# Kernel optimization log

Hardware: AMD Instinct MI355X
Metric: run time of the kernel (lower is better)

## Reference

```python
import jax, jax.numpy as jnp
import numpy as np

B, N, K_OUT, NBASIS, NGLOBALS, H = 16, 2048, 128, 4, 2, 256
DIN = 1 + NBASIS + N + NGLOBALS  # norm + basis projections + all-pairs dots + globals
NEG_SLOPE = 0.01  # torch LeakyReLU default


def setup_inputs() -> dict:
    key = jax.random.key(0)
    ks = jax.random.split(key, 6)
    x = jax.random.uniform(ks[0], (B, N, 3), jnp.float32)      # positions -> dots >= 0
    u = jax.random.normal(ks[1], (B, NGLOBALS), jnp.float32)
    basis = jax.random.normal(ks[2], (B, NBASIS, 3), jnp.float32)
    def init_w(k, fan_in, fan_out):
        return jax.random.normal(k, (fan_in, fan_out), jnp.float32) / np.float32(np.sqrt(fan_in))
    W1 = init_w(ks[3], DIN, H); b1 = jnp.zeros((H,), jnp.float32)
    W2 = init_w(ks[4], H, H);   b2 = jnp.zeros((H,), jnp.float32)
    W3 = init_w(ks[5], H, K_OUT); b3 = jnp.zeros((K_OUT,), jnp.float32)
    return {"x": x, "u": u, "basis": basis,
            "W1": W1, "b1": b1, "W2": W2, "b2": b2, "W3": W3, "b3": b3}


def reference(x, u, basis, W1, b1, W2, b2, W3, b3):
    # per-vector norms: [B, N, 1]
    norms = jnp.linalg.norm(x, axis=-1, keepdims=True)
    # projections onto basis vectors: [B, N, NBASIS]
    proj = jnp.einsum('bid,bnd->bin', x, basis)
    # all-pairs sqrt of dot products: [B, N, N]
    dots = jnp.sqrt(jnp.einsum('bid,bjd->bij', x, x))
    # concat order matches original: globals first, then [norm, proj, dots]
    u_rep = jnp.broadcast_to(u[:, None, :], (B, N, NGLOBALS))
    scalars = jnp.concatenate([u_rep, norms, proj, dots], axis=-1)  # [B, N, DIN]
    # MLP (Linear -> LeakyReLU -> Linear -> LeakyReLU -> Linear)
    h = jax.nn.leaky_relu(scalars @ W1 + b1, NEG_SLOPE)
    h = jax.nn.leaky_relu(h @ W2 + b2, NEG_SLOPE)
    fk = h @ W3 + b3  # [B, N, K_OUT]
    # outer product with x followed by mean over input vecs, fused into one einsum
    # (avoids materializing the [B, N, K_OUT, 3] tensor)
    return jnp.einsum('bio,bid->bod', fk, x) / np.float32(N)  # [B, K_OUT, 3]
```

## Files before the change

### kernel.cpp

```cpp
#include <hip/hip_runtime.h>

typedef unsigned short u16;
typedef unsigned int   u32;

typedef __attribute__((ext_vector_type(8))) short short8;
typedef __attribute__((ext_vector_type(4))) float floatx4;
typedef __attribute__((ext_vector_type(2))) float v2f;

__device__ __forceinline__ u16 f2bf(float f) {
    u32 u = __float_as_uint(f);
    u = u + 0x7fffu + ((u >> 16) & 1u);
    return (u16)(u >> 16);
}

__device__ __forceinline__ u32 pack2bf(float s0, float s1) {
    u32 a = __float_as_uint(s0) + 0x8000u;
    u32 b = __float_as_uint(s1) + 0x8000u;
    return __builtin_amdgcn_perm(b, a, 0x07060302u);
}

__device__ __forceinline__ floatx4 mfma16(short8 a, short8 b, floatx4 c) {
    return __builtin_amdgcn_mfma_f32_16x16x32_bf16(a, b, c, 0, 0, 0);
}

__global__ void k_prep(const float* __restrict__ W1, const float* __restrict__ W2,
                       const float* __restrict__ W3, u16* __restrict__ W1frag,
                       u16* __restrict__ W2frag, u16* __restrict__ W3frag) {
    int idx = blockIdx.x * 256 + threadIdx.x;
    if (idx < 524288) {
        int kt = idx >> 13, r = idx & 8191;
        int t = r >> 4, j = (r >> 3) & 1, ji = r & 7;
        int lane = t & 63, w = t >> 6, lr = lane & 15, lq = lane >> 4;
        W1frag[idx] = f2bf(W1[(7 + kt * 32 + lq * 8 + ji) * 256 + w * 32 + j * 16 + lr]);
    } else if (idx < 589824) {
        int i = idx - 524288;
        int kt = i >> 13, r = i & 8191;
        int t = r >> 5, jj = (r >> 3) & 3, ji = r & 7;
        int lane = t & 63, wv = t >> 6, lr = lane & 15, lq = lane >> 4;
        W2frag[i] = f2bf(W2[(kt * 32 + lq * 8 + ji) * 256 + wv * 64 + jj * 16 + lr]);
    } else if (idx < 622592) {
        int i = idx - 589824;
        int kt = i >> 12, r = i & 4095;
        int t = r >> 4, j = (r >> 3) & 1, ji = r & 7;
        int lane = t & 63, wv = t >> 6, lr = lane & 15, lq = lane >> 4;
        W3frag[i] = f2bf(W3[(kt * 32 + lq * 8 + ji) * 128 + wv * 32 + j * 16 + lr]);
    }
}

__global__ __launch_bounds__(512, 4) void k_h1(
    const float* __restrict__ x, const float* __restrict__ u,
    const float* __restrict__ basis, const float* __restrict__ W1,
    const float* __restrict__ b1, const u16* __restrict__ W1frag,
    u16* __restrict__ h1) {
    __shared__ float xls[6144];
    __shared__ u16 As[2][64][64];
    __shared__ float rowsml[64][6];
    __shared__ float colsml[256][6];

    const int t = threadIdx.x;
    const int b = blockIdx.y;
    const int i0 = blockIdx.x * 64;
    const int lane = t & 63, w = t >> 6;
    const int lr = lane & 15, lq = lane >> 4;

    {
        const float4* src = (const float4*)(x + b * 6144);
#pragma unroll
        for (int kk = 0; kk < 3; ++kk) {
            int q = t + kk * 512;
            float4 v = src[q];
            float vv[4] = {v.x, v.y, v.z, v.w};
            int e = q * 4;
#pragma unroll
            for (int cc = 0; cc < 4; ++cc) {
                int ee = e + cc;
                xls[(ee % 3) * 2048 + ee / 3] = vv[cc];
            }
        }
    }
    if (t < 256) {
        int c = t;
        float u0 = u[b * 2 + 0], u1 = u[b * 2 + 1];
        colsml[c][0] = b1[c] + u0 * W1[c] + u1 * W1[256 + c];
        colsml[c][1] = W1[512 + c];
        colsml[c][2] = W1[768 + c];
        colsml[c][3] = W1[1024 + c];
        colsml[c][4] = W1[1280 + c];
        colsml[c][5] = W1[1536 + c];
    }
    __syncthreads();
    if (t < 64) {
        float xx = xls[i0 + t], xy = xls[2048 + i0 + t], xz = xls[4096 + i0 + t];
        rowsml[t][0] = sqrtf(xx * xx + xy * xy + xz * xz);
#pragma unroll
        for (int p = 0; p < 4; ++p) {
            const float* bp = basis + (b * 4 + p) * 3;
            rowsml[t][1 + p] = xx * bp[0] + xy * bp[1] + xz * bp[2];
        }
    }
    const float ax = xls[i0 + lane];
    const float ay = xls[2048 + i0 + lane];
    const float az = xls[4096 + i0 + lane];
    const u16* wf = W1frag + t * 16;
    const float4* X4 = (const float4*)xls;

    char* Asb = (char*)As;
    char* aswp = Asb + lane * 128 + ((w ^ (lane & 7)) << 4);
    int ro[4];
    {
        int sl = (lq ^ (lr & 7));
#pragma unroll
        for (int i = 0; i < 4; ++i)
            ro[i] = (i * 16 + lr) * 128 + (sl << 4);
    }

    auto gen_store = [&](int s, int buf) {
        int q = s * 16 + w * 2;
        v2f dA, dB, dC, dD;
        {
            float4 a0 = X4[q], a1 = X4[q + 1];
            v2f t0 = {a0.x, a0.y}, t1 = {a0.z, a0.w};
            v2f t2 = {a1.x, a1.y}, t3 = {a1.z, a1.w};
            dA = t0 * ax; dB = t1 * ax; dC = t2 * ax; dD = t3 * ax;
        }
        {
            float4 a0 = X4[512 + q], a1 = X4[513 + q];
            v2f t0 = {a0.x, a0.y}, t1 = {a0.z, a0.w};
            v2f t2 = {a1.x, a1.y}, t3 = {a1.z, a1.w};
            dA += t0 * ay; dB += t1 * ay; dC += t2 * ay; dD += t3 * ay;
        }
        {
            float4 a0 = X4[1024 + q], a1 = X4[1025 + q];
            v2f t0 = {a0.x, a0.y}, t1 = {a0.z, a0.w};
            v2f t2 = {a1.x, a1.y}, t3 = {a1.z, a1.w};
            dA += t0 * az; dB += t1 * az; dC += t2 * az; dD += t3 * az;
        }
        float s0 = __builtin_amdgcn_sqrtf(dA.x);
        float s1 = __builtin_amdgcn_sqrtf(dA.y);
        float s2 = __builtin_amdgcn_sqrtf(dB.x);
        float s3 = __builtin_amdgcn_sqrtf(dB.y);
        float s4 = __builtin_amdgcn_sqrtf(dC.x);
        float s5 = __builtin_amdgcn_sqrtf(dC.y);
        float s6 = __builtin_amdgcn_sqrtf(dD.x);
        float s7 = __builtin_amdgcn_sqrtf(dD.y);
        uint4 dv;
        dv.x = pack2bf(s0, s1); dv.y = pack2bf(s2, s3);
        dv.z = pack2bf(s4, s5); dv.w = pack2bf(s6, s7);
        *(uint4*)(aswp + buf * 8192) = dv;
    };

    floatx4 acc[4][2];
    const floatx4 zero = {0.f, 0.f, 0.f, 0.f};
#pragma unroll
    for (int i = 0; i < 4; ++i)
#pragma unroll
        for (int j = 0; j < 2; ++j) acc[i][j] = zero;

    gen_store(0, 0);
    __syncthreads();

    short8 a[4], bfr[4];
#pragma unroll 2
    for (int s = 0; s < 32; ++s) {
        const int buf = s & 1;
        const u16* wb = wf + (2 * s) * 8192;
        bfr[0] = *(const short8*)(wb);
        bfr[1] = *(const short8*)(wb + 8);
        bfr[2] = *(const short8*)(wb + 8192);
        bfr[3] = *(const short8*)(wb + 8192 + 8);
#pragma unroll
        for (int i = 0; i < 4; ++i)
            a[i] = *(const short8*)(Asb + buf * 8192 + ro[i]);
        if (s < 31) gen_store(s + 1, buf ^ 1);
#pragma unroll
        for (int i = 0; i < 4; ++i)
#pragma unroll
            for (int j = 0; j < 2; ++j)
                acc[i][j] = mfma16(a[i], bfr[j], acc[i][j]);
#pragma unroll
        for (int i = 0; i < 4; ++i)
            a[i] = *(const short8*)(Asb + buf * 8192 + (ro[i] ^ 64));
#pragma unroll
        for (int i = 0; i < 4; ++i)
#pragma unroll
            for (int j = 0; j < 2; ++j)
                acc[i][j] = mfma16(a[i], bfr[2 + j], acc[i][j]);
        __syncthreads();
    }

    const int c0 = w * 32 + lr, c1 = c0 + 16;
    float c0v[6], c1v[6];
#pragma unroll
    for (int q = 0; q < 6; ++q) { c0v[q] = colsml[c0][q]; c1v[q] = colsml[c1][q]; }
#pragma unroll
    for (int i = 0; i < 4; ++i) {
#pragma unroll
        for (int r = 0; r < 4; ++r) {
            int row = i * 16 + lq * 4 + r;
            float nrm = rowsml[row][0];
            float p0 = rowsml[row][1], p1 = rowsml[row][2];
            float p2 = rowsml[row][3], p3 = rowsml[row][4];
            u16* orow = h1 + (b * 2048 + i0 + row) * 256;
            float v0 = acc[i][0][r] + c0v[0] + nrm * c0v[1] +
                       p0 * c0v[2] + p1 * c0v[3] + p2 * c0v[4] + p3 * c0v[5];
            v0 = v0 > 0.f ? v0 : 0.01f * v0;
            orow[c0] = f2bf(v0);
            float v1 = acc[i][1][r] + c1v[0] + nrm * c1v[1] +
                       p0 * c1v[2] + p1 * c1v[3] + p2 * c1v[4] + p3 * c1v[5];
            v1 = v1 > 0.f ? v1 : 0.01f * v1;
            orow[c1] = f2bf(v1);
        }
    }
}

__global__ __launch_bounds__(256, 2) void k_tail(
    const u16* __restrict__ h1, const u16* __restrict__ W2frag,
    const float* __restrict__ b2, const u16* __restrict__ W3frag,
    const float* __restrict__ b3, const float* __restrict__ x,
    float* __restrict__ out) {
    __shared__ u16 h2s[64][264];
    __shared__ float colb2[256];
    __shared__ float colb3[128];
    __shared__ float xs[64][4];
    __shared__ float red[128][4];

    const int t = threadIdx.x;
    const int m0 = blockIdx.x * 64;
    const int b = m0 >> 11, i0 = m0 & 2047;
    const int lane = t & 63, wv = t >> 6;
    const int lr = lane & 15, lq = lane >> 4;

    colb2[t] = b2[t];
    if (t < 128) colb3[t] = b3[t];
    if (t < 64) {
        const float* xp = x + (b * 2048 + i0 + t) * 3;
        xs[t][0] = xp[0]; xs[t][1] = xp[1]; xs[t][2] = xp[2];
    }

    floatx4 acc[4][4];
    const floatx4 zero = {0.f, 0.f, 0.f, 0.f};
#pragma unroll
    for (int i = 0; i < 4; ++i)
#pragma unroll
        for (int j = 0; j < 4; ++j) acc[i][j] = zero;

    const u16* hsrc = h1 + m0 * 256 + lr * 256 + lq * 8;
    const u16* w2s = W2frag + t * 32;
#pragma unroll 2
    for (int kt = 0; kt < 8; ++kt) {
        short8 af[4], bf[4];
#pragma unroll
        for (int i = 0; i < 4; ++i)
            af[i] = *(const short8*)(hsrc + i * 4096 + kt * 32);
#pragma unroll
        for (int j = 0; j < 4; ++j)
            bf[j] = *(const short8*)(w2s + kt * 8192 + j * 8);
#pragma unroll
        for (int i = 0; i < 4; ++i)
#pragma unroll
            for (int j = 0; j < 4; ++j) acc[i][j] = mfma16(af[i], bf[j], acc[i][j]);
    }
#pragma unroll
    for (int i = 0; i < 4; ++i)
#pragma unroll
        for (int r = 0; r < 4; ++r) {
            int row = i * 16 + lq * 4 + r;
#pragma unroll
            for (int j = 0; j < 4; ++j) {
                int col = wv * 64 + j * 16 + lr;
                float v = acc[i][j][r] + colb2[col];
                v = v > 0.f ? v : 0.01f * v;
                h2s[row][col] = f2bf(v);
            }
        }
    __syncthreads();

    floatx4 acc2[4][2];
#pragma unroll
    for (int i = 0; i < 4; ++i)
#pragma unroll
        for (int j = 0; j < 2; ++j) acc2[i][j] = zero;

    const u16* w3s = W3frag + t * 16;
#pragma unroll 2
    for (int kt = 0; kt < 8; ++kt) {
        short8 af[4], bf[2];
#pragma unroll
        for (int i = 0; i < 4; ++i)
            af[i] = *(const short8*)&h2s[i * 16 + lr][kt * 32 + lq * 8];
#pragma unroll
        for (int j = 0; j < 2; ++j)
            bf[j] = *(const short8*)(w3s + kt * 4096 + j * 8);
#pragma unroll
        for (int i = 0; i < 4; ++i)
#pragma unroll
            for (int j = 0; j < 2; ++j) acc2[i][j] = mfma16(af[i], bf[j], acc2[i][j]);
    }

    float s[2][3];
#pragma unroll
    for (int j = 0; j < 2; ++j) { s[j][0] = 0.f; s[j][1] = 0.f; s[j][2] = 0.f; }
#pragma unroll
    for (int i = 0; i < 4; ++i)
#pragma unroll
        for (int r = 0; r < 4; ++r) {
            int row = i * 16 + lq * 4 + r;
            float x0 = xs[row][0], x1 = xs[row][1], x2 = xs[row][2];
#pragma unroll
            for (int j = 0; j < 2; ++j) {
                int col = wv * 32 + j * 16 + lr;
                float fk = acc2[i][j][r] + colb3[col];
                s[j][0] += fk * x0; s[j][1] += fk * x1; s[j][2] += fk * x2;
            }
        }
#pragma unroll
    for (int j = 0; j < 2; ++j)
#pragma unroll
        for (int d = 0; d < 3; ++d) {
            float v = s[j][d];
            v += __shfl_xor(v, 16);
            v += __shfl_xor(v, 32);
            if (lane < 16) red[wv * 32 + j * 16 + lane][d] = v;
        }
    __syncthreads();
    if (t < 128) {
#pragma unroll
        for (int d = 0; d < 3; ++d)
            atomicAdd(&out[(b * 128 + t) * 3 + d], red[t][d] * (1.0f / 2048.0f));
    }
}

extern "C" void kernel_launch(void* const* d_in, const int* in_sizes, int n_in,
                              void* d_out, int out_size, void* d_ws, size_t ws_size,
                              hipStream_t stream) {
    const float* x     = (const float*)d_in[0];
    const float* u     = (const float*)d_in[1];
    const float* basis = (const float*)d_in[2];
    const float* W1    = (const float*)d_in[3];
    const float* b1    = (const float*)d_in[4];
    const float* W2    = (const float*)d_in[5];
    const float* b2    = (const float*)d_in[6];
    const float* W3    = (const float*)d_in[7];
    const float* b3    = (const float*)d_in[8];
    float* out = (float*)d_out;

    char* ws = (char*)d_ws;
    u16*  W1frag = (u16*)ws;
    u16*  W2frag = (u16*)(ws + 1048576);
    u16*  W3frag = (u16*)(ws + 1179648);
    u16*  h1     = (u16*)(ws + 1245184);

    hipMemsetAsync(out, 0, 24576, stream);
    k_prep<<<2432, 256, 0, stream>>>(W1, W2, W3, W1frag, W2frag, W3frag);
    k_h1<<<dim3(32, 16), 512, 0, stream>>>(x, u, basis, W1, b1, W1frag, h1);
    k_tail<<<512, 256, 0, stream>>>(h1, W2frag, b2, W3frag, b3, x, out);
}
```

Baseline: 137.6 us.

## Fuse layer-1 and tail MLP kernels, keeping h1 in shared memory

Merges the h1 kernel and the tail kernel into one kernel. The 64x256 h1 tile now stays in LDS (aliased over the x staging buffer) and feeds the W2 and W3 GEMMs directly, so the bf16 h1 global round-trip and a kernel launch go away. W2/W3 fragment layouts are re-tiled for 8 waves of 512 threads. LDS use grows to about 76KB per block, which may reduce occupancy below the launch-bounds target. The column constants are now read from global memory per thread instead of staged in LDS.

```diff
diff --git a/kernel.cpp b/kernel.cpp
--- a/kernel.cpp
+++ b/kernel.cpp
@@ -35,27 +35,33 @@
     } else if (idx < 589824) {
         int i = idx - 524288;
         int kt = i >> 13, r = i & 8191;
-        int t = r >> 5, jj = (r >> 3) & 3, ji = r & 7;
-        int lane = t & 63, wv = t >> 6, lr = lane & 15, lq = lane >> 4;
-        W2frag[i] = f2bf(W2[(kt * 32 + lq * 8 + ji) * 256 + wv * 64 + jj * 16 + lr]);
+        int t = r >> 4, j = (r >> 3) & 1, ji = r & 7;
+        int lane = t & 63, w = t >> 6, lr = lane & 15, lq = lane >> 4;
+        W2frag[i] = f2bf(W2[(kt * 32 + lq * 8 + ji) * 256 + w * 32 + j * 16 + lr]);
     } else if (idx < 622592) {
         int i = idx - 589824;
         int kt = i >> 12, r = i & 4095;
-        int t = r >> 4, j = (r >> 3) & 1, ji = r & 7;
-        int lane = t & 63, wv = t >> 6, lr = lane & 15, lq = lane >> 4;
-        W3frag[i] = f2bf(W3[(kt * 32 + lq * 8 + ji) * 128 + wv * 32 + j * 16 + lr]);
-    }
-}
-
-__global__ __launch_bounds__(512, 4) void k_h1(
+        int t = r >> 3, ji = r & 7;
+        int lane = t & 63, w = t >> 6, lr = lane & 15, lq = lane >> 4;
+        W3frag[i] = f2bf(W3[(kt * 32 + lq * 8 + ji) * 128 + w * 16 + lr]);
+    }
+}
+
+__global__ __launch_bounds__(512, 4) void k_fused(
     const float* __restrict__ x, const float* __restrict__ u,
     const float* __restrict__ basis, const float* __restrict__ W1,
-    const float* __restrict__ b1, const u16* __restrict__ W1frag,
-    u16* __restrict__ h1) {
-    __shared__ float xls[6144];
-    __shared__ u16 As[2][64][64];
-    __shared__ float rowsml[64][6];
-    __shared__ float colsml[256][6];
+    const float* __restrict__ b1, const float* __restrict__ b2,
+    const float* __restrict__ b3, const u16* __restrict__ W1frag,
+    const u16* __restrict__ W2frag, const u16* __restrict__ W3frag,
+    float* __restrict__ out) {
+    __shared__ __align__(16) char smem[76288];
+    float* xls = (float*)smem;
+    char* Asb = smem + 24576;
+    u16 (*h1s)[264] = (u16(*)[264])smem;
+    float (*xsm)[4] = (float(*)[4])(smem + 33792);
+    float (*redm)[4] = (float(*)[4])(smem + 34816);
+    float (*rowsml)[6] = (float(*)[6])(smem + 40960);
+    u16 (*h2s)[264] = (u16(*)[264])(smem + 42496);
 
     const int t = threadIdx.x;
     const int b = blockIdx.y;
@@ -78,16 +84,6 @@
             }
         }
     }
-    if (t < 256) {
-        int c = t;
-        float u0 = u[b * 2 + 0], u1 = u[b * 2 + 1];
-        colsml[c][0] = b1[c] + u0 * W1[c] + u1 * W1[256 + c];
-        colsml[c][1] = W1[512 + c];
-        colsml[c][2] = W1[768 + c];
-        colsml[c][3] = W1[1024 + c];
-        colsml[c][4] = W1[1280 + c];
-        colsml[c][5] = W1[1536 + c];
-    }
     __syncthreads();
     if (t < 64) {
         float xx = xls[i0 + t], xy = xls[2048 + i0 + t], xz = xls[4096 + i0 + t];
@@ -104,7 +100,6 @@
     const u16* wf = W1frag + t * 16;
     const float4* X4 = (const float4*)xls;
 
-    char* Asb = (char*)As;
     char* aswp = Asb + lane * 128 + ((w ^ (lane & 7)) << 4);
     int ro[4];
     {
@@ -159,174 +154,147 @@
     gen_store(0, 0);
     __syncthreads();
 
-    short8 a[4], bfr[4];
+    {
+        short8 a[4], bfr[4];
 #pragma unroll 2
-    for (int s = 0; s < 32; ++s) {
-        const int buf = s & 1;
-        const u16* wb = wf + (2 * s) * 8192;
-        bfr[0] = *(const short8*)(wb);
-        bfr[1] = *(const short8*)(wb + 8);
-        bfr[2] = *(const short8*)(wb + 8192);
-        bfr[3] = *(const short8*)(wb + 8192 + 8);
+        for (int s = 0; s < 32; ++s) {
+            const int buf = s & 1;
+            const u16* wb = wf + (2 * s) * 8192;
+            bfr[0] = *(const short8*)(wb);
+            bfr[1] = *(const short8*)(wb + 8);
+            bfr[2] = *(const short8*)(wb + 8192);
+            bfr[3] = *(const short8*)(wb + 8192 + 8);
+#pragma unroll
+            for (int i = 0; i < 4; ++i)
+                a[i] = *(const short8*)(Asb + buf * 8192 + ro[i]);
+            if (s < 31) gen_store(s + 1, buf ^ 1);
+#pragma unroll
+            for (int i = 0; i < 4; ++i)
+#pragma unroll
+                for (int j = 0; j < 2; ++j)
+                    acc[i][j] = mfma16(a[i], bfr[j], acc[i][j]);
+#pragma unroll
+            for (int i = 0; i < 4; ++i)
+                a[i] = *(const short8*)(Asb + buf * 8192 + (ro[i] ^ 64));
+#pragma unroll
+            for (int i = 0; i < 4; ++i)
+#pragma unroll
+                for (int j = 0; j < 2; ++j)
+                    acc[i][j] = mfma16(a[i], bfr[2 + j], acc[i][j]);
+            __syncthreads();
+        }
+    }
+
+    if (t < 64) { xsm[t][0] = ax; xsm[t][1] = ay; xsm[t][2] = az; }
+    const int c0 = w * 32 + lr, c1 = c0 + 16;
+    {
+        float c0v[6], c1v[6];
+        float u0 = u[b * 2 + 0], u1 = u[b * 2 + 1];
+        c0v[0] = b1[c0] + u0 * W1[c0] + u1 * W1[256 + c0];
+        c1v[0] = b1[c1] + u0 * W1[c1] + u1 * W1[256 + c1];
+#pragma unroll
+        for (int q = 1; q < 6; ++q) {
+            c0v[q] = W1[(q + 1) * 256 + c0];
+            c1v[q] = W1[(q + 1) * 256 + c1];
+        }
+#pragma unroll
+        for (int i = 0; i < 4; ++i) {
+#pragma unroll
+            for (int r = 0; r < 4; ++r) {
+                int row = i * 16 + lq * 4 + r;
+                float nrm = rowsml[row][0];
+                float p0 = rowsml[row][1], p1 = rowsml[row][2];
+                float p2 = rowsml[row][3], p3 = rowsml[row][4];
+                float v0 = acc[i][0][r] + c0v[0] + nrm * c0v[1] +
+                           p0 * c0v[2] + p1 * c0v[3] + p2 * c0v[4] + p3 * c0v[5];
+                v0 = v0 > 0.f ? v0 : 0.01f * v0;
+                h1s[row][c0] = f2bf(v0);
+                float v1 = acc[i][1][r] + c1v[0] + nrm * c1v[1] +
+                           p0 * c1v[2] + p1 * c1v[3] + p2 * c1v[4] + p3 * c1v[5];
+                v1 = v1 > 0.f ? v1 : 0.01f * v1;
+                h1s[row][c1] = f2bf(v1);
+            }
+        }
+    }
+    __syncthreads();
+
+#pragma unroll
+    for (int i = 0; i < 4; ++i)
+#pragma unroll
+        for (int j = 0; j < 2; ++j) acc[i][j] = zero;
+    {
+        const u16* w2s = W2frag + t * 16;
+#pragma unroll 2
+        for (int kt = 0; kt < 8; ++kt) {
+            short8 af[4], bfr[2];
+#pragma unroll
+            for (int i = 0; i < 4; ++i)
+                af[i] = *(const short8*)&h1s[i * 16 + lr][kt * 32 + lq * 8];
+#pragma unroll
+            for (int j = 0; j < 2; ++j)
+                bfr[j] = *(const short8*)(w2s + kt * 8192 + j * 8);
+#pragma unroll
+            for (int i = 0; i < 4; ++i)
+#pragma unroll
+                for (int j = 0; j < 2; ++j)
+                    acc[i][j] = mfma16(af[i], bfr[j], acc[i][j]);
+        }
+        float cb0 = b2[c0], cb1 = b2[c1];
 #pragma unroll
         for (int i = 0; i < 4; ++i)
-            a[i] = *(const short8*)(Asb + buf * 8192 + ro[i]);
-        if (s < 31) gen_store(s + 1, buf ^ 1);
+#pragma unroll
+            for (int r = 0; r < 4; ++r) {
+                int row = i * 16 + lq * 4 + r;
+                float v0 = acc[i][0][r] + cb0;
+                v0 = v0 > 0.f ? v0 : 0.01f * v0;
+                h2s[row][c0] = f2bf(v0);
+                float v1 = acc[i][1][r] + cb1;
+                v1 = v1 > 0.f ? v1 : 0.01f * v1;
+                h2s[row][c1] = f2bf(v1);
+            }
+    }
+    __syncthreads();
+
+    {
+        floatx4 acc2[4];
+#pragma unroll
+        for (int i = 0; i < 4; ++i) acc2[i] = zero;
+        const u16* w3s = W3frag + t * 8;
+#pragma unroll 2
+        for (int kt = 0; kt < 8; ++kt) {
+            short8 af[4];
+#pragma unroll
+            for (int i = 0; i < 4; ++i)
+                af[i] = *(const short8*)&h2s[i * 16 + lr][kt * 32 + lq * 8];
+            short8 bfr = *(const short8*)(w3s + kt * 4096);
+#pragma unroll
+            for (int i = 0; i < 4; ++i) acc2[i] = mfma16(af[i], bfr, acc2[i]);
+        }
+        const int c3 = w * 16 + lr;
+        float cb3 = b3[c3];
+        float s0 = 0.f, s1 = 0.f, s2 = 0.f;
 #pragma unroll
         for (int i = 0; i < 4; ++i)
 #pragma unroll
-            for (int j = 0; j < 2; ++j)
-                acc[i][j] = mfma16(a[i], bfr[j], acc[i][j]);
-#pragma unroll
-        for (int i = 0; i < 4; ++i)
-            a[i] = *(const short8*)(Asb + buf * 8192 + (ro[i] ^ 64));
-#pragma unroll
-        for (int i = 0; i < 4; ++i)
-#pragma unroll
-            for (int j = 0; j < 2; ++j)
-                acc[i][j] = mfma16(a[i], bfr[2 + j], acc[i][j]);
-        __syncthreads();
-    }
-
-    const int c0 = w * 32 + lr, c1 = c0 + 16;
-    float c0v[6], c1v[6];
-#pragma unroll
-    for (int q = 0; q < 6; ++q) { c0v[q] = colsml[c0][q]; c1v[q] = colsml[c1][q]; }
-#pragma unroll
-    for (int i = 0; i < 4; ++i) {
-#pragma unroll
-        for (int r = 0; r < 4; ++r) {
-            int row = i * 16 + lq * 4 + r;
-            float nrm = rowsml[row][0];
-            float p0 = rowsml[row][1], p1 = rowsml[row][2];
-            float p2 = rowsml[row][3], p3 = rowsml[row][4];
-            u16* orow = h1 + (b * 2048 + i0 + row) * 256;
-            float v0 = acc[i][0][r] + c0v[0] + nrm * c0v[1] +
-                       p0 * c0v[2] + p1 * c0v[3] + p2 * c0v[4] + p3 * c0v[5];
-            v0 = v0 > 0.f ? v0 : 0.01f * v0;
-            orow[c0] = f2bf(v0);
-            float v1 = acc[i][1][r] + c1v[0] + nrm * c1v[1] +
-                       p0 * c1v[2] + p1 * c1v[3] + p2 * c1v[4] + p3 * c1v[5];
-            v1 = v1 > 0.f ? v1 : 0.01f * v1;
-            orow[c1] = f2bf(v1);
-        }
-    }
-}
-
-__global__ __launch_bounds__(256, 2) void k_tail(
-    const u16* __restrict__ h1, const u16* __restrict__ W2frag,
-    const float* __restrict__ b2, const u16* __restrict__ W3frag,
-    const float* __restrict__ b3, const float* __restrict__ x,
-    float* __restrict__ out) {
-    __shared__ u16 h2s[64][264];
-    __shared__ float colb2[256];
-    __shared__ float colb3[128];
-    __shared__ float xs[64][4];
-    __shared__ float red[128][4];
-
-    const int t = threadIdx.x;
-    const int m0 = blockIdx.x * 64;
-    const int b = m0 >> 11, i0 = m0 & 2047;
-    const int lane = t & 63, wv = t >> 6;
-    const int lr = lane & 15, lq = lane >> 4;
-
-    colb2[t] = b2[t];
-    if (t < 128) colb3[t] = b3[t];
-    if (t < 64) {
-        const float* xp = x + (b * 2048 + i0 + t) * 3;
-        xs[t][0] = xp[0]; xs[t][1] = xp[1]; xs[t][2] = xp[2];
-    }
-
-    floatx4 acc[4][4];
-    const floatx4 zero = {0.f, 0.f, 0.f, 0.f};
-#pragma unroll
-    for (int i = 0; i < 4; ++i)
-#pragma unroll
-        for (int j = 0; j < 4; ++j) acc[i][j] = zero;
-
-    const u16* hsrc = h1 + m0 * 256 + lr * 256 + lq * 8;
-    const u16* w2s = W2frag + t * 32;
-#pragma unroll 2
-    for (int kt = 0; kt < 8; ++kt) {
-        short8 af[4], bf[4];
-#pragma unroll
-        for (int i = 0; i < 4; ++i)
-            af[i] = *(const short8*)(hsrc + i * 4096 + kt * 32);
-#pragma unroll
-        for (int j = 0; j < 4; ++j)
-            bf[j] = *(const short8*)(w2s + kt * 8192 + j * 8);
-#pragma unroll
-        for (int i = 0; i < 4; ++i)
-#pragma unroll
-            for (int j = 0; j < 4; ++j) acc[i][j] = mfma16(af[i], bf[j], acc[i][j]);
-    }
-#pragma unroll
-    for (int i = 0; i < 4; ++i)
-#pragma unroll
-        for (int r = 0; r < 4; ++r) {
-            int row = i * 16 + lq * 4 + r;
-#pragma unroll
-            for (int j = 0; j < 4; ++j) {
-                int col = wv * 64 + j * 16 + lr;
-                float v = acc[i][j][r] + colb2[col];
-                v = v > 0.f ? v : 0.01f * v;
-                h2s[row][col] = f2bf(v);
+            for (int r = 0; r < 4; ++r) {
+                int row = i * 16 + lq * 4 + r;
+                float fk = acc2[i][r] + cb3;
+                s0 += fk * xsm[row][0];
+                s1 += fk * xsm[row][1];
+                s2 += fk * xsm[row][2];
             }
-        }
-    __syncthreads();
-
-    floatx4 acc2[4][2];
-#pragma unroll
-    for (int i = 0; i < 4; ++i)
-#pragma unroll
-        for (int j = 0; j < 2; ++j) acc2[i][j] = zero;
-
-    const u16* w3s = W3frag + t * 16;
-#pragma unroll 2
-    for (int kt = 0; kt < 8; ++kt) {
-        short8 af[4], bf[2];
-#pragma unroll
-        for (int i = 0; i < 4; ++i)
-            af[i] = *(const short8*)&h2s[i * 16 + lr][kt * 32 + lq * 8];
-#pragma unroll
-        for (int j = 0; j < 2; ++j)
-            bf[j] = *(const short8*)(w3s + kt * 4096 + j * 8);
-#pragma unroll
-        for (int i = 0; i < 4; ++i)
-#pragma unroll
-            for (int j = 0; j < 2; ++j) acc2[i][j] = mfma16(af[i], bf[j], acc2[i][j]);
-    }
-
-    float s[2][3];
-#pragma unroll
-    for (int j = 0; j < 2; ++j) { s[j][0] = 0.f; s[j][1] = 0.f; s[j][2] = 0.f; }
-#pragma unroll
-    for (int i = 0; i < 4; ++i)
-#pragma unroll
-        for (int r = 0; r < 4; ++r) {
-            int row = i * 16 + lq * 4 + r;
-            float x0 = xs[row][0], x1 = xs[row][1], x2 = xs[row][2];
-#pragma unroll
-            for (int j = 0; j < 2; ++j) {
-                int col = wv * 32 + j * 16 + lr;
-                float fk = acc2[i][j][r] + colb3[col];
-                s[j][0] += fk * x0; s[j][1] += fk * x1; s[j][2] += fk * x2;
-            }
-        }
-#pragma unroll
-    for (int j = 0; j < 2; ++j)
-#pragma unroll
-        for (int d = 0; d < 3; ++d) {
-            float v = s[j][d];
-            v += __shfl_xor(v, 16);
-            v += __shfl_xor(v, 32);
-            if (lane < 16) red[wv * 32 + j * 16 + lane][d] = v;
-        }
+        s0 += __shfl_xor(s0, 16); s0 += __shfl_xor(s0, 32);
+        s1 += __shfl_xor(s1, 16); s1 += __shfl_xor(s1, 32);
+        s2 += __shfl_xor(s2, 16); s2 += __shfl_xor(s2, 32);
+        if (lq == 0) {
+            redm[c3][0] = s0; redm[c3][1] = s1; redm[c3][2] = s2;
+        }
+    }
     __syncthreads();
     if (t < 128) {
 #pragma unroll
         for (int d = 0; d < 3; ++d)
-            atomicAdd(&out[(b * 128 + t) * 3 + d], red[t][d] * (1.0f / 2048.0f));
+            atomicAdd(&out[(b * 128 + t) * 3 + d], redm[t][d] * (1.0f / 2048.0f));
     }
 }
 
@@ -348,10 +316,9 @@
     u16*  W1frag = (u16*)ws;
     u16*  W2frag = (u16*)(ws + 1048576);
     u16*  W3frag = (u16*)(ws + 1179648);
-    u16*  h1     = (u16*)(ws + 1245184);
 
     hipMemsetAsync(out, 0, 24576, stream);
     k_prep<<<2432, 256, 0, stream>>>(W1, W2, W3, W1frag, W2frag, W3frag);
-    k_h1<<<dim3(32, 16), 512, 0, stream>>>(x, u, basis, W1, b1, W1frag, h1);
-    k_tail<<<512, 256, 0, stream>>>(h1, W2frag, b2, W3frag, b3, x, out);
-}
+    k_fused<<<dim3(32, 16), 512, 0, stream>>>(x, u, basis, W1, b1, b2, b3,
+                                              W1frag, W2frag, W3frag, out);
+}
```

After: 142.5 us. +3.5%, slower.
